# Kernel optimization log

Hardware: AMD Instinct MI355X
Metric: run time of the kernel (lower is better)

## Reference

```python
import jax, jax.numpy as jnp
import numpy as np

B, C, H, W, D = 8, 3, 256, 320, 64
IDEPTH_BASE = 1.0 / 50.0
IDEPTH_STEP = (1.0 / 0.5 - 1.0 / 50.0) / 63.0


def _camera_geometry():
    # Mirrors DepthProjectionModule.getValue's numpy math (assumes 640x480 source frames).
    pix = np.indices([W, H]).astype(np.float32)            # [2, 320, 256]  (u, v)
    pix = np.concatenate([pix, np.ones([1, W, H], np.float32)], 0).reshape(3, -1)  # [3, N]
    left_pose = np.asarray([[0.07543147, 0.61393189, -0.78574661, 1.3405],
                            [0.9970987, -0.03837025, 0.06574118, 0.6266],
                            [0.01021131, -0.78842588, -0.61504501, 1.6575],
                            [0, 0, 0, 1]])
    right_pose = np.asarray([[0.0640527011, 0.640832173, -0.765004168, 1.316],
                             [0.997946496, -0.0409736058, 0.0492336713, 0.6254],
                             [0.000205541383, -0.766586779, -0.642140692, 1.6196],
                             [0, 0, 0, 1]])
    K = np.asarray([[525.0, 0, 319.5], [0, 525.0, 239.5], [0, 0, 1]])
    K[0, :] *= W / 640.0
    K[1, :] *= H / 480.0
    l2r = np.linalg.inv(right_pose) @ left_pose
    Rm, t = l2r[:3, :3], l2r[:3, 3]
    KRKi = K @ Rm @ np.linalg.inv(K)
    KRKiUV = (KRKi @ pix).astype(np.float32)               # [3, N]
    KT = (K @ t).astype(np.float32).reshape(3, 1)          # [3, 1]
    return KRKiUV, KT


def setup_inputs() -> dict:
    key = jax.random.key(0)
    k1, k2 = jax.random.split(key)
    left_image = jax.random.normal(k1, (B, C, H, W), jnp.float32)
    right_image = jax.random.normal(k2, (B, C, H, W), jnp.float32)
    KRKiUV, KT = _camera_geometry()
    KRKiUV_T = jnp.broadcast_to(jnp.asarray(KRKiUV)[None], (B, 3, W * H))
    KT_T = jnp.broadcast_to(jnp.asarray(KT)[None], (B, 3, 1))
    return {"left_image": left_image, "right_image": right_image,
            "KRKiUV_T": KRKiUV_T, "KT_T": KT_T}


def _grid_sample_bilinear_zeros(img, gx, gy):
    # img: [B,C,H,W]; gx, gy: [B,D,H,W] in [-1,1]; align_corners=True, zeros padding.
    ix = (gx + 1.0) * 0.5 * (W - 1)
    iy = (gy + 1.0) * 0.5 * (H - 1)
    x0 = jnp.floor(ix)
    y0 = jnp.floor(iy)
    wx1 = ix - x0
    wy1 = iy - y0
    imgf = img.reshape(img.shape[0], img.shape[1], H * W)

    def gather(f, idx):  # f: [C,HW], idx: [D,H,W] -> [C,D,H,W]
        return jnp.take(f, idx.reshape(-1), axis=1).reshape(f.shape[0], D, H, W)

    def corner(xc, yc, w):
        valid = (xc >= 0) & (xc <= W - 1) & (yc >= 0) & (yc <= H - 1)
        xi = jnp.clip(xc, 0, W - 1).astype(jnp.int32)
        yi = jnp.clip(yc, 0, H - 1).astype(jnp.int32)
        g = jax.vmap(gather)(imgf, yi * W + xi)            # [B,C,D,H,W]
        return g * (w * valid)[:, None]                    # broadcast over C

    return (corner(x0, y0, (1 - wx1) * (1 - wy1))
            + corner(x0 + 1, y0, wx1 * (1 - wy1))
            + corner(x0, y0 + 1, (1 - wx1) * wy1)
            + corner(x0 + 1, y0 + 1, wx1 * wy1))           # [B,C,D,H,W]


def reference(left_image, right_image, KRKiUV_T, KT_T):
    depths = 1.0 / (IDEPTH_BASE + jnp.arange(D, dtype=jnp.float32) * IDEPTH_STEP)  # [D]
    # transformed: [B,D,3,N]
    transformed = KRKiUV_T[:, None] * depths[None, :, None, None] + KT_T[:, None]
    warp_uv = transformed[:, :, 0:2] / (transformed[:, :, 2:3] + 1e-6)             # [B,D,2,N]
    base = jnp.asarray([W / 2.0, H / 2.0], jnp.float32).reshape(1, 1, 2, 1)
    warp_uv = (warp_uv - base) / base
    # view(B,D,2,W,H) then permute -> [B,D,H,W,2]
    grid = warp_uv.reshape(B, D, 2, W, H).transpose(0, 1, 4, 3, 2)
    warped = _grid_sample_bilinear_zeros(right_image, grid[..., 0], grid[..., 1])  # [B,C,D,H,W]
    costvolume = jnp.sum(jnp.abs(warped - left_image[:, :, None]), axis=1)         # [B,D,H,W]
    return costvolume
```

## Files before the change

### kernel.cpp

```cpp
#include <hip/hip_runtime.h>
#include <hip/hip_fp16.h>
#include <math.h>

#define Wd 320
#define Hd 256
#define Bd 8
#define Cd 3
#define Dd 64
#define HWd (Hd * Wd)
#define DT 2


__global__ __launch_bounds__(256) void pack_f16(const float* __restrict__ right,
                                                const float* __restrict__ left,
                                                uint4* __restrict__ ws) {
    const int p = blockIdx.x * 256 + threadIdx.x;
    const int plane = blockIdx.y;
    const int c = plane % Cd;
    const float* src = (plane < Cd ? right : left) + (size_t)c * HWd + p;
    unsigned w[4];
#pragma unroll
    for (int k = 0; k < 4; ++k) {
        const float f0 = src[(size_t)(2 * k) * (Cd * HWd)];
        const float f1 = src[(size_t)(2 * k + 1) * (Cd * HWd)];
        const __half2 h = __halves2half2(__float2half_rn(f0), __float2half_rn(f1));
        w[k] = __builtin_bit_cast(unsigned, h);
    }
    ws[(size_t)plane * HWd + p] = make_uint4(w[0], w[1], w[2], w[3]);
}

__global__ __launch_bounds__(256) void costvol_kernel(
    const uint4* __restrict__ ws,
    float* __restrict__ out,
    double a00, double a01, double a02,
    double a10, double a11, double a12,
    double a20, double a21, double a22,
    float kt0, float kt1, float kt2)
{
    const int q = blockIdx.x * 256 + threadIdx.x;
    const int d0 = blockIdx.y * DT;
    const int x = q % Wd;
    const int y = q / Wd;

    const float k0 = (float)(a00 * (double)x + a01 * (double)y + a02);
    const float k1 = (float)(a10 * (double)x + a11 * (double)y + a12);
    const float k2 = (float)(a20 * (double)x + a21 * (double)y + a22);

    uint4 lv[Cd];
#pragma unroll
    for (int c = 0; c < Cd; ++c) lv[c] = ws[(size_t)(Cd + c) * HWd + q];

    const float base  = (float)(1.0 / 50.0);
    const float stepf = (float)((1.0 / 0.5 - 1.0 / 50.0) / 63.0);

#pragma unroll
    for (int dd = 0; dd < DT; ++dd) {
        const int d = d0 + dd;

        const float depth = 1.0f / (base + (float)d * stepf);

        const float tx = k0 * depth + kt0;
        const float ty = k1 * depth + kt1;
        const float tz = k2 * depth + kt2;

        const float den = tz + 1e-6f;
        const float u = tx / den;
        const float v = ty / den;

        const float gx = (u - (float)(Wd / 2)) / (float)(Wd / 2);
        const float gy = (v - (float)(Hd / 2)) / (float)(Hd / 2);
        const float ix = (gx + 1.0f) * 0.5f * (float)(Wd - 1);
        const float iy = (gy + 1.0f) * 0.5f * (float)(Hd - 1);

        const float x0f = floorf(ix);
        const float y0f = floorf(iy);
        const float wx1 = ix - x0f;
        const float wy1 = iy - y0f;
        const float wx0 = 1.0f - wx1;
        const float wy0 = 1.0f - wy1;
        const float x1f = x0f + 1.0f;
        const float y1f = y0f + 1.0f;

        const float vx0 = (x0f >= 0.0f && x0f <= (float)(Wd - 1)) ? 1.0f : 0.0f;
        const float vx1 = (x1f >= 0.0f && x1f <= (float)(Wd - 1)) ? 1.0f : 0.0f;
        const float vy0 = (y0f >= 0.0f && y0f <= (float)(Hd - 1)) ? 1.0f : 0.0f;
        const float vy1 = (y1f >= 0.0f && y1f <= (float)(Hd - 1)) ? 1.0f : 0.0f;

        const float w00 = wx0 * wy0 * (vx0 * vy0);
        const float w10 = wx1 * wy0 * (vx1 * vy0);
        const float w01 = wx0 * wy1 * (vx0 * vy1);
        const float w11 = wx1 * wy1 * (vx1 * vy1);

        const int xi0 = (int)fminf(fmaxf(x0f, 0.0f), (float)(Wd - 1));
        const int xi1 = (int)fminf(fmaxf(x1f, 0.0f), (float)(Wd - 1));
        const int yi0 = (int)fminf(fmaxf(y0f, 0.0f), (float)(Hd - 1));
        const int yi1 = (int)fminf(fmaxf(y1f, 0.0f), (float)(Hd - 1));

        const int i00 = yi0 * Wd + xi0;
        const int i10 = yi0 * Wd + xi1;
        const int i01 = yi1 * Wd + xi0;
        const int i11 = yi1 * Wd + xi1;

        const __half2 w00p = __half2half2(__float2half_rn(w00));
        const __half2 w10p = __half2half2(__float2half_rn(w10));
        const __half2 w01p = __half2half2(__float2half_rn(w01));
        const __half2 w11p = __half2half2(__float2half_rn(w11));

        __half2 acc[4];
#pragma unroll
        for (int k = 0; k < 4; ++k) acc[k] = __half2half2(__float2half_rn(0.0f));

#pragma unroll
        for (int c = 0; c < Cd; ++c) {
            const uint4* rc = ws + (size_t)c * HWd;
            const uint4 g00 = rc[i00];
            const uint4 g10 = rc[i10];
            const uint4 g01 = rc[i01];
            const uint4 g11 = rc[i11];

            const unsigned* u00 = (const unsigned*)&g00;
            const unsigned* u10 = (const unsigned*)&g10;
            const unsigned* u01 = (const unsigned*)&g01;
            const unsigned* u11 = (const unsigned*)&g11;
            const unsigned* ul  = (const unsigned*)&lv[c];

#pragma unroll
            for (int k = 0; k < 4; ++k) {
                const __half2 h00 = __builtin_bit_cast(__half2, u00[k]);
                const __half2 h10 = __builtin_bit_cast(__half2, u10[k]);
                const __half2 h01 = __builtin_bit_cast(__half2, u01[k]);
                const __half2 h11 = __builtin_bit_cast(__half2, u11[k]);
                const __half2 hl  = __builtin_bit_cast(__half2, ul[k]);
                __half2 wrp = __hfma2(w00p, h00,
                              __hfma2(w10p, h10,
                              __hfma2(w01p, h01,
                              __hmul2(w11p, h11))));
                const __half2 df = __habs2(__hsub2(wrp, hl));
                acc[k] = __hadd2(acc[k], df);
            }
        }

        const int out_off = d * HWd + q;
#pragma unroll
        for (int k = 0; k < 4; ++k) {
            const float lo = __low2float(acc[k]);
            const float hi = __high2float(acc[k]);
            __builtin_nontemporal_store(lo, &out[(size_t)(2 * k) * (Dd * HWd) + out_off]);
            __builtin_nontemporal_store(hi, &out[(size_t)(2 * k + 1) * (Dd * HWd) + out_off]);
        }
    }
}


static void invert4(const double A[4][4], double inv[4][4]) {
    double M[4][8];
    for (int i = 0; i < 4; ++i) {
        for (int j = 0; j < 4; ++j) { M[i][j] = A[i][j]; M[i][j + 4] = (i == j) ? 1.0 : 0.0; }
    }
    for (int col = 0; col < 4; ++col) {
        int piv = col;
        for (int r = col + 1; r < 4; ++r)
            if (fabs(M[r][col]) > fabs(M[piv][col])) piv = r;
        if (piv != col)
            for (int j = 0; j < 8; ++j) { double t = M[col][j]; M[col][j] = M[piv][j]; M[piv][j] = t; }
        const double p = M[col][col];
        for (int j = 0; j < 8; ++j) M[col][j] /= p;
        for (int r = 0; r < 4; ++r) if (r != col) {
            const double f = M[r][col];
            for (int j = 0; j < 8; ++j) M[r][j] -= f * M[col][j];
        }
    }
    for (int i = 0; i < 4; ++i)
        for (int j = 0; j < 4; ++j) inv[i][j] = M[i][j + 4];
}

static void mul4(const double A[4][4], const double B[4][4], double C[4][4]) {
    for (int i = 0; i < 4; ++i)
        for (int j = 0; j < 4; ++j) {
            double s = 0.0;
            for (int k = 0; k < 4; ++k) s += A[i][k] * B[k][j];
            C[i][j] = s;
        }
}

static void mul3(const double A[3][3], const double B[3][3], double C[3][3]) {
    for (int i = 0; i < 3; ++i)
        for (int j = 0; j < 3; ++j) {
            double s = 0.0;
            for (int k = 0; k < 3; ++k) s += A[i][k] * B[k][j];
            C[i][j] = s;
        }
}

extern "C" void kernel_launch(void* const* d_in, const int* in_sizes, int n_in,
                              void* d_out, int out_size, void* d_ws, size_t ws_size,
                              hipStream_t stream) {
    const float* left  = (const float*)d_in[0];
    const float* right = (const float*)d_in[1];
    float* out = (float*)d_out;
    uint4* ws = (uint4*)d_ws;

    const double LP[4][4] = {
        {0.07543147, 0.61393189, -0.78574661, 1.3405},
        {0.9970987, -0.03837025, 0.06574118, 0.6266},
        {0.01021131, -0.78842588, -0.61504501, 1.6575},
        {0.0, 0.0, 0.0, 1.0}};
    const double RP[4][4] = {
        {0.0640527011, 0.640832173, -0.765004168, 1.316},
        {0.997946496, -0.0409736058, 0.0492336713, 0.6254},
        {0.000205541383, -0.766586779, -0.642140692, 1.6196},
        {0.0, 0.0, 0.0, 1.0}};
    double K[3][3] = {{525.0, 0.0, 319.5}, {0.0, 525.0, 239.5}, {0.0, 0.0, 1.0}};
    for (int j = 0; j < 3; ++j) K[0][j] *= (double)Wd / 640.0;
    for (int j = 0; j < 3; ++j) K[1][j] *= (double)Hd / 480.0;

    double iRP[4][4];
    invert4(RP, iRP);
    double l2r[4][4];
    mul4(iRP, LP, l2r);

    double Rm[3][3], t[3];
    for (int i = 0; i < 3; ++i) {
        for (int j = 0; j < 3; ++j) Rm[i][j] = l2r[i][j];
        t[i] = l2r[i][3];
    }

    const double iK[3][3] = {
        {1.0 / K[0][0], 0.0, -K[0][2] / K[0][0]},
        {0.0, 1.0 / K[1][1], -K[1][2] / K[1][1]},
        {0.0, 0.0, 1.0}};

    double T1[3][3], KRKi[3][3];
    mul3(K, Rm, T1);
    mul3(T1, iK, KRKi);

    double Ktd[3] = {0.0, 0.0, 0.0};
    for (int i = 0; i < 3; ++i)
        for (int k = 0; k < 3; ++k) Ktd[i] += K[i][k] * t[k];
    const float kt0 = (float)Ktd[0], kt1 = (float)Ktd[1], kt2 = (float)Ktd[2];

    {
        dim3 grid(HWd / 256, 2 * Cd, 1);
        pack_f16<<<grid, dim3(256), 0, stream>>>(right, left, ws);
    }

    {
        dim3 grid(HWd / 256, Dd / DT, 1);
        costvol_kernel<<<grid, dim3(256), 0, stream>>>(
            ws, out,
            KRKi[0][0], KRKi[0][1], KRKi[0][2],
            KRKi[1][0], KRKi[1][1], KRKi[1][2],
            KRKi[2][0], KRKi[2][1], KRKi[2][2],
            kt0, kt1, kt2);
    }
}
```

Measured before the change: 56.81 us.

## Pack horizontal pixel pairs per entry and read left image directly

```diff
diff --git a/kernel.cpp b/kernel.cpp
--- a/kernel.cpp
+++ b/kernel.cpp
@@ -8,29 +8,53 @@
 #define Cd 3
 #define Dd 64
 #define HWd (Hd * Wd)
-#define DT 2
-
-
-__global__ __launch_bounds__(256) void pack_f16(const float* __restrict__ right,
-                                                const float* __restrict__ left,
-                                                uint4* __restrict__ ws) {
-    const int p = blockIdx.x * 256 + threadIdx.x;
+#define DT 4
+#define BOFF (HWd / 2)
+#define PSZ (HWd + 1)
+#define GUARD 164
+
+
+static __device__ __forceinline__ unsigned pk2(float a, float b) {
+    return __builtin_bit_cast(unsigned, __halves2half2(__float2half_rn(a), __float2half_rn(b)));
+}
+
+__global__ __launch_bounds__(256) void pack_right(const float* __restrict__ right,
+                                                  uint4* __restrict__ ws4) {
+    const int j = blockIdx.x * 256 + threadIdx.x;
     const int plane = blockIdx.y;
+    if (plane == 6) {
+        if (blockIdx.x == 0 && threadIdx.x < GUARD)
+            ws4[threadIdx.x] = make_uint4(0u, 0u, 0u, 0u);
+        return;
+    }
+    const int g = plane / Cd;
     const int c = plane % Cd;
-    const float* src = (plane < Cd ? right : left) + (size_t)c * HWd + p;
-    unsigned w[4];
-#pragma unroll
-    for (int k = 0; k < 4; ++k) {
-        const float f0 = src[(size_t)(2 * k) * (Cd * HWd)];
-        const float f1 = src[(size_t)(2 * k + 1) * (Cd * HWd)];
-        const __half2 h = __halves2half2(__float2half_rn(f0), __float2half_rn(f1));
-        w[k] = __builtin_bit_cast(unsigned, h);
-    }
-    ws[(size_t)plane * HWd + p] = make_uint4(w[0], w[1], w[2], w[3]);
+    const int b0 = g * 4;
+    const int p0 = 2 * j;
+    const int p2 = (p0 + 2 < HWd) ? (p0 + 2) : (HWd - 1);
+    float f0[4], f1[4], f2[4];
+#pragma unroll
+    for (int i = 0; i < 4; ++i) {
+        const float* sp = right + ((size_t)(b0 + i) * Cd + c) * HWd;
+        f0[i] = sp[p0];
+        f1[i] = sp[p0 + 1];
+        f2[i] = sp[p2];
+    }
+    const unsigned a0 = pk2(f0[0], f0[1]);
+    const unsigned a1 = pk2(f0[2], f0[3]);
+    const unsigned b1 = pk2(f1[0], f1[1]);
+    const unsigned b2 = pk2(f1[2], f1[3]);
+    uint4* pbase = ws4 + GUARD + (size_t)plane * PSZ;
+    pbase[j] = make_uint4(a0, a1, b1, b2);
+    pbase[BOFF + 1 + j] = make_uint4(b1, b2, pk2(f2[0], f2[1]),
+                                     pk2(f2[2], f2[3]));
+    if (j == 0)
+        pbase[BOFF] = make_uint4(a0, a1, a0, a1);
 }
 
 __global__ __launch_bounds__(256) void costvol_kernel(
-    const uint4* __restrict__ ws,
+    const float* __restrict__ left,
+    const uint4* __restrict__ ws4,
     float* __restrict__ out,
     double a00, double a01, double a02,
     double a10, double a11, double a12,
@@ -46,10 +70,17 @@
     const float k1 = (float)(a10 * (double)x + a11 * (double)y + a12);
     const float k2 = (float)(a20 * (double)x + a21 * (double)y + a22);
 
-    uint4 lv[Cd];
-#pragma unroll
-    for (int c = 0; c < Cd; ++c) lv[c] = ws[(size_t)(Cd + c) * HWd + q];
-
+    __half2 hlp[Cd][4];
+#pragma unroll
+    for (int c = 0; c < Cd; ++c)
+#pragma unroll
+        for (int k = 0; k < 4; ++k) {
+            const float l0 = left[((size_t)(2 * k) * Cd + c) * HWd + q];
+            const float l1 = left[((size_t)(2 * k + 1) * Cd + c) * HWd + q];
+            hlp[c][k] = __halves2half2(__float2half_rn(l0), __float2half_rn(l1));
+        }
+
+    const uint4* rp = ws4 + GUARD;
     const float base  = (float)(1.0 / 50.0);
     const float stepf = (float)((1.0 / 0.5 - 1.0 / 50.0) / 63.0);
 
@@ -91,15 +122,12 @@
         const float w01 = wx0 * wy1 * (vx0 * vy1);
         const float w11 = wx1 * wy1 * (vx1 * vy1);
 
-        const int xi0 = (int)fminf(fmaxf(x0f, 0.0f), (float)(Wd - 1));
-        const int xi1 = (int)fminf(fmaxf(x1f, 0.0f), (float)(Wd - 1));
-        const int yi0 = (int)fminf(fmaxf(y0f, 0.0f), (float)(Hd - 1));
-        const int yi1 = (int)fminf(fmaxf(y1f, 0.0f), (float)(Hd - 1));
-
-        const int i00 = yi0 * Wd + xi0;
-        const int i10 = yi0 * Wd + xi1;
-        const int i01 = yi1 * Wd + xi0;
-        const int i11 = yi1 * Wd + xi1;
+        const int xb = (int)fminf(fmaxf(x0f, -1.0f), (float)(Wd - 1));
+        const int yb = (int)fminf(fmaxf(y0f, -1.0f), (float)(Hd - 1));
+        const int ibase = yb * Wd + xb;
+        const int m = ibase >> 1;
+        const int entry = (xb & 1) ? (BOFF + 1 + m) : m;
+        const int roffp = (yb < Hd - 1) ? (Wd / 2) : 0;
 
         const __half2 w00p = __half2half2(__float2half_rn(w00));
         const __half2 w10p = __half2half2(__float2half_rn(w10));
@@ -111,32 +139,28 @@
         for (int k = 0; k < 4; ++k) acc[k] = __half2half2(__float2half_rn(0.0f));
 
 #pragma unroll
-        for (int c = 0; c < Cd; ++c) {
-            const uint4* rc = ws + (size_t)c * HWd;
-            const uint4 g00 = rc[i00];
-            const uint4 g10 = rc[i10];
-            const uint4 g01 = rc[i01];
-            const uint4 g11 = rc[i11];
-
-            const unsigned* u00 = (const unsigned*)&g00;
-            const unsigned* u10 = (const unsigned*)&g10;
-            const unsigned* u01 = (const unsigned*)&g01;
-            const unsigned* u11 = (const unsigned*)&g11;
-            const unsigned* ul  = (const unsigned*)&lv[c];
-
-#pragma unroll
-            for (int k = 0; k < 4; ++k) {
-                const __half2 h00 = __builtin_bit_cast(__half2, u00[k]);
-                const __half2 h10 = __builtin_bit_cast(__half2, u10[k]);
-                const __half2 h01 = __builtin_bit_cast(__half2, u01[k]);
-                const __half2 h11 = __builtin_bit_cast(__half2, u11[k]);
-                const __half2 hl  = __builtin_bit_cast(__half2, ul[k]);
-                __half2 wrp = __hfma2(w00p, h00,
-                              __hfma2(w10p, h10,
-                              __hfma2(w01p, h01,
-                              __hmul2(w11p, h11))));
-                const __half2 df = __habs2(__hsub2(wrp, hl));
-                acc[k] = __hadd2(acc[k], df);
+        for (int g = 0; g < 2; ++g) {
+#pragma unroll
+            for (int c = 0; c < Cd; ++c) {
+                const uint4* pl = rp + (size_t)(g * Cd + c) * PSZ;
+                const uint4 r0 = pl[entry];
+                const uint4 r1 = pl[entry + roffp];
+                const unsigned* u0 = (const unsigned*)&r0;
+                const unsigned* u1 = (const unsigned*)&r1;
+#pragma unroll
+                for (int k = 0; k < 2; ++k) {
+                    const __half2 h00 = __builtin_bit_cast(__half2, u0[k]);
+                    const __half2 h10 = __builtin_bit_cast(__half2, u0[k + 2]);
+                    const __half2 h01 = __builtin_bit_cast(__half2, u1[k]);
+                    const __half2 h11 = __builtin_bit_cast(__half2, u1[k + 2]);
+                    const __half2 hl  = hlp[c][g * 2 + k];
+                    __half2 wrp = __hfma2(w00p, h00,
+                                  __hfma2(w10p, h10,
+                                  __hfma2(w01p, h01,
+                                  __hmul2(w11p, h11))));
+                    const __half2 df = __habs2(__hsub2(wrp, hl));
+                    acc[g * 2 + k] = __hadd2(acc[g * 2 + k], df);
+                }
             }
         }
 
@@ -198,7 +222,7 @@
     const float* left  = (const float*)d_in[0];
     const float* right = (const float*)d_in[1];
     float* out = (float*)d_out;
-    uint4* ws = (uint4*)d_ws;
+    uint4* ws4 = (uint4*)d_ws;
 
     const double LP[4][4] = {
         {0.07543147, 0.61393189, -0.78574661, 1.3405},
@@ -240,14 +264,14 @@
     const float kt0 = (float)Ktd[0], kt1 = (float)Ktd[1], kt2 = (float)Ktd[2];
 
     {
-        dim3 grid(HWd / 256, 2 * Cd, 1);
-        pack_f16<<<grid, dim3(256), 0, stream>>>(right, left, ws);
+        dim3 grid(BOFF / 256, 7, 1);
+        pack_right<<<grid, dim3(256), 0, stream>>>(right, ws4);
     }
 
     {
         dim3 grid(HWd / 256, Dd / DT, 1);
         costvol_kernel<<<grid, dim3(256), 0, stream>>>(
-            ws, out,
+            left, ws4, out,
             KRKi[0][0], KRKi[0][1], KRKi[0][2],
             KRKi[1][0], KRKi[1][1], KRKi[1][2],
             KRKi[2][0], KRKi[2][1], KRKi[2][2],
```

New measurement: 80.78 us. +42.2%, slower.
